# Kernel tuning notes

Measured on AMD Instinct MI355X. Metric: run time of the kernel, lower is better.

The kernel has to match this reference:

```python
import jax, jax.numpy as jnp
import numpy as np

N_NODES = 100000
N_EDGES = 640000
EMB = 128
BATCH = 16384
N_REL = 2
HIDDEN = [128, 64, 32]
LN_EPS = 1e-5
NORM_EPS = 1e-12


def setup_inputs() -> dict:
    key = jax.random.key(0)
    ks = jax.random.split(key, 24)
    inp = {}
    inp["user_indices"] = jax.random.randint(ks[0], (BATCH,), 0, N_NODES)
    inp["item_indices"] = jax.random.randint(ks[1], (BATCH,), 0, N_NODES)
    inp["edge_index"] = jax.random.randint(ks[2], (2, N_EDGES), 0, N_NODES)
    inp["edge_type"] = jax.random.randint(ks[3], (N_EDGES,), 0, N_REL)
    inp["edge_weight"] = jax.random.uniform(ks[4], (N_EDGES,), dtype=jnp.float32)
    # parameters
    s = 1.0 / np.sqrt(EMB)
    inp["embedding"] = jax.random.normal(ks[5], (N_NODES, EMB), jnp.float32) * 0.02
    inp["w1_rel"] = jax.random.normal(ks[6], (N_REL, EMB, EMB), jnp.float32) * s
    inp["w1_root"] = jax.random.normal(ks[7], (EMB, EMB), jnp.float32) * s
    inp["b1"] = jnp.zeros((EMB,), jnp.float32)
    inp["ln_g"] = jnp.ones((EMB,), jnp.float32)
    inp["ln_b"] = jnp.zeros((EMB,), jnp.float32)
    inp["w2_rel"] = jax.random.normal(ks[8], (N_REL, EMB, EMB), jnp.float32) * s
    inp["w2_root"] = jax.random.normal(ks[9], (EMB, EMB), jnp.float32) * s
    inp["b2"] = jnp.zeros((EMB,), jnp.float32)
    dims = [2 * EMB] + HIDDEN
    for i in range(len(HIDDEN)):
        inp[f"mlp_w{i}"] = jax.random.normal(ks[10 + i], (dims[i], dims[i + 1]), jnp.float32) / np.sqrt(dims[i])
        inp[f"mlp_b{i}"] = jnp.zeros((dims[i + 1],), jnp.float32)
    d_out = HIDDEN[-1] + EMB
    inp["out_w"] = jax.random.normal(ks[20], (d_out, 1), jnp.float32) / np.sqrt(d_out)
    inp["out_b"] = jnp.zeros((1,), jnp.float32)
    return inp


def rgcn_layer(x, edge_index, edge_type, edge_weight, w_rel, w_root, bias):
    # x: [N, D]; edge_index: [2, E]; per-relation linear on gathered source feats,
    # weighted scatter-add into destination nodes, plus root transform + bias.
    src, dst = edge_index[0], edge_index[1]
    x_j = x[src]  # [E, D] gather
    msg = jnp.zeros((x_j.shape[0], w_rel.shape[2]), x.dtype)
    for r in range(w_rel.shape[0]):  # small fixed relation count
        msg = msg + jnp.where((edge_type == r)[:, None], x_j @ w_rel[r], 0.0)
    msg = msg * edge_weight[:, None]
    agg = jax.ops.segment_sum(msg, dst, num_segments=x.shape[0])
    return agg + x @ w_root + bias


def layer_norm(x, g, b):
    mu = jnp.mean(x, axis=-1, keepdims=True)
    var = jnp.mean(jnp.square(x - mu), axis=-1, keepdims=True)
    return (x - mu) * jax.lax.rsqrt(var + LN_EPS) * g + b


def l2_normalize(x):
    n = jnp.sqrt(jnp.sum(jnp.square(x), axis=-1, keepdims=True))
    return x / jnp.maximum(n, NORM_EPS)


def reference(user_indices, item_indices, edge_index, edge_type, edge_weight,
              embedding, w1_rel, w1_root, b1, ln_g, ln_b, w2_rel, w2_root, b2,
              mlp_w0, mlp_b0, mlp_w1, mlp_b1, mlp_w2, mlp_b2, out_w, out_b):
    x = embedding  # embedding(arange(N)) == full table
    x = rgcn_layer(x, edge_index, edge_type, edge_weight, w1_rel, w1_root, b1)
    x = jax.nn.relu(x)
    # dropout is identity in eval mode
    x = layer_norm(x, ln_g, ln_b)
    x = rgcn_layer(x, edge_index, edge_type, edge_weight, w2_rel, w2_root, b2)

    u = x[user_indices]  # [B, D]
    v = x[item_indices]
    gmf = l2_normalize(u) * l2_normalize(v)  # [B, D]
    h = jnp.concatenate([u, v], axis=-1)  # [B, 2D]
    for w, b in ((mlp_w0, mlp_b0), (mlp_w1, mlp_b1), (mlp_w2, mlp_b2)):
        h = jax.nn.relu(h @ w + b)
    final = jnp.concatenate([gmf, h], axis=-1)  # [B, D + 32]
    score = jax.nn.sigmoid(final @ out_w + out_b)
    return jnp.squeeze(score, axis=-1)
```

## Files before the change

kernel.cpp:

```cpp
#include <hip/hip_runtime.h>
#include <cstddef>
#include <cstdint>

#define N_NODES 100000
#define N_EDGES 640000
#define EMBD    128
#define NBATCH  16384
#define CHUNK   1024
#define NCHUNK  ((N_NODES + CHUNK - 1) / CHUNK)

typedef short bf16x8 __attribute__((ext_vector_type(8)));
typedef float f32x4  __attribute__((ext_vector_type(4)));

__device__ __forceinline__ unsigned pack_split(float x) {
    unsigned u  = __float_as_uint(x);
    unsigned hi = (u + 0x7fffu + ((u >> 16) & 1u)) & 0xffff0000u;
    float    lo = x - __uint_as_float(hi);
    unsigned ul = __float_as_uint(lo);
    unsigned lw = ((ul + 0x7fffu + ((ul >> 16) & 1u)) >> 16) & 0xffffu;
    return hi | lw;
}
__device__ __forceinline__ float unpack_split(unsigned u) {
    return __uint_as_float(u & 0xffff0000u) + __uint_as_float(u << 16);
}
__device__ __forceinline__ float bf2f(unsigned short h) {
    return __uint_as_float((unsigned)h << 16);
}

__global__ __launch_bounds__(256) void pack_hist(
    const float* __restrict__ emb, unsigned* __restrict__ xp,
    unsigned short* __restrict__ xh,
    const int* __restrict__ ei, int* __restrict__ cursor, int n2, int E)
{
    const int j = blockIdx.x * 256 + threadIdx.x;
    if (j < n2) {
        const float2 v = ((const float2*)emb)[j];
        const unsigned p0 = pack_split(v.x);
        const unsigned p1 = pack_split(v.y);
        ((uint2*)xp)[j] = make_uint2(p0, p1);
        if (xh) ((unsigned*)xh)[j] = (p0 >> 16) | (p1 & 0xffff0000u);
    }
    if (j < E) atomicAdd(&cursor[ei[E + j]], 1);
}

__global__ __launch_bounds__(256) void scan_local(
    int* __restrict__ cursor, int* __restrict__ bsum, int n)
{
    __shared__ int part[256];
    const int t    = threadIdx.x;
    const int base = blockIdx.x * CHUNK + t * 4;
    int v[4];
    int s = 0;
#pragma unroll
    for (int i = 0; i < 4; ++i) {
        const int idx = base + i;
        v[i] = (idx < n) ? cursor[idx] : 0;
        s += v[i];
    }
    part[t] = s;
    __syncthreads();
    for (int off = 1; off < 256; off <<= 1) {
        const int add = (t >= off) ? part[t - off] : 0;
        __syncthreads();
        part[t] += add;
        __syncthreads();
    }
    if (t == 255) bsum[blockIdx.x] = part[255];
    int run = (t == 0) ? 0 : part[t - 1];
#pragma unroll
    for (int i = 0; i < 4; ++i) {
        const int idx = base + i;
        if (idx < n) { cursor[idx] = run; run += v[i]; }
    }
}

__global__ __launch_bounds__(256) void scan_add(
    int* __restrict__ cursor, const int* __restrict__ bsum, int n)
{
    __shared__ int red[256];
    const int t = threadIdx.x;
    const int b = blockIdx.x;
    red[t] = (t < b && t < NCHUNK) ? bsum[t] : 0;
    __syncthreads();
    for (int off = 128; off > 0; off >>= 1) {
        if (t < off) red[t] += red[t + off];
        __syncthreads();
    }
    const int off_ = red[0];
    const int base = b * CHUNK + t * 4;
#pragma unroll
    for (int i = 0; i < 4; ++i) {
        const int idx = base + i;
        if (idx < n) cursor[idx] += off_;
    }
}

__global__ __launch_bounds__(256) void bucket_kernel(
    const int* __restrict__ ei, const int* __restrict__ et,
    const float* __restrict__ ew, int* __restrict__ cursor,
    int2* __restrict__ srec, int E)
{
    const int e = blockIdx.x * 256 + threadIdx.x;
    if (e >= E) return;
    const int src = ei[e];
    const int dst = ei[E + e];
    const int r   = et[e];
    const int pos = atomicAdd(&cursor[dst], 1);
    srec[pos] = make_int2(src | (r << 17), __float_as_int(ew[e]));
}

template <bool HI>
__global__ __launch_bounds__(256) void accum_csr(
    const unsigned* __restrict__ xp, const unsigned short* __restrict__ xh,
    const int2* __restrict__ srec, const int* __restrict__ cursor,
    unsigned* __restrict__ Ap, int N)
{
    const int wid  = blockIdx.x * 4 + (threadIdx.x >> 6);
    const int lane = threadIdx.x & 63;
    const int s = (wid == 0) ? 0 : cursor[wid - 1];
    const int e = cursor[wid];

    float ax = 0.f, ay = 0.f, bx = 0.f, by = 0.f;

    auto fetch = [&](int src, float& vx, float& vy) {
        if (HI) {
            const unsigned g = ((const unsigned*)(xh + (size_t)src * EMBD))[lane];
            vx = bf2f((unsigned short)(g & 0xffffu));
            vy = bf2f((unsigned short)(g >> 16));
        } else {
            const uint2 g = ((const uint2*)(xp + (size_t)src * EMBD))[lane];
            vx = unpack_split(g.x);
            vy = unpack_split(g.y);
        }
    };

    int i = s;
    for (; i + 3 < e; i += 4) {
        const int2 r0 = srec[i];
        const int2 r1 = srec[i + 1];
        const int2 r2 = srec[i + 2];
        const int2 r3 = srec[i + 3];
        float x0, y0, x1, y1, x2v, y2v, x3, y3;
        fetch(r0.x & 0x1FFFF, x0, y0);
        fetch(r1.x & 0x1FFFF, x1, y1);
        fetch(r2.x & 0x1FFFF, x2v, y2v);
        fetch(r3.x & 0x1FFFF, x3, y3);
        const float w0 = __int_as_float(r0.y);
        const float w1 = __int_as_float(r1.y);
        const float w2 = __int_as_float(r2.y);
        const float w3 = __int_as_float(r3.y);
        if (r0.x & (1 << 17)) { bx += x0 * w0;  by += y0 * w0; }
        else                  { ax += x0 * w0;  ay += y0 * w0; }
        if (r1.x & (1 << 17)) { bx += x1 * w1;  by += y1 * w1; }
        else                  { ax += x1 * w1;  ay += y1 * w1; }
        if (r2.x & (1 << 17)) { bx += x2v * w2; by += y2v * w2; }
        else                  { ax += x2v * w2; ay += y2v * w2; }
        if (r3.x & (1 << 17)) { bx += x3 * w3;  by += y3 * w3; }
        else                  { ax += x3 * w3;  ay += y3 * w3; }
    }
    for (; i < e; ++i) {
        const int2 r0 = srec[i];
        float x0, y0;
        fetch(r0.x & 0x1FFFF, x0, y0);
        const float w0 = __int_as_float(r0.y);
        if (r0.x & (1 << 17)) { bx += x0 * w0; by += y0 * w0; }
        else                  { ax += x0 * w0; ay += y0 * w0; }
    }
    ((uint2*)(Ap + (size_t)wid * EMBD))[lane]       = make_uint2(pack_split(ax), pack_split(ay));
    ((uint2*)(Ap + ((size_t)N + wid) * EMBD))[lane] = make_uint2(pack_split(bx), pack_split(by));
}

__global__ __launch_bounds__(256) void gemm_mfma(
    const unsigned* __restrict__ S0, const unsigned* __restrict__ S1,
    const unsigned* __restrict__ S2,
    const float* __restrict__ wrel, const float* __restrict__ wroot,
    const float* __restrict__ bias, const float* __restrict__ lng,
    const float* __restrict__ lnb, void* __restrict__ outv,
    unsigned short* __restrict__ ohi,
    int M, int do_ln)
{
    __shared__ unsigned short AsH[128 * 40], AsL[128 * 40];
    __shared__ unsigned short BsH[128 * 40], BsL[128 * 40];
    __shared__ float lnbuf[2][128][2];

    const int t    = threadIdx.x;
    const int wave = t >> 6;
    const int lane = t & 63;
    const int q    = lane >> 4;
    const int n    = lane & 15;
    const int wrow = wave & 1;
    const int wcol = wave >> 1;
    const int m0   = blockIdx.x * 128;

    const int arow  = t >> 1;
    const int ahalf = t & 1;
    const int bcol  = t & 127;
    const int bkh   = t >> 7;

    f32x4 acc[4][4];
#pragma unroll
    for (int rt = 0; rt < 4; ++rt)
#pragma unroll
        for (int ct = 0; ct < 4; ++ct)
            acc[rt][ct] = (f32x4){0.f, 0.f, 0.f, 0.f};

    uint4 au0, au1, au2, au3;
    auto loadA = [&](int kc) {
        const unsigned* Sp = (kc < 4) ? S0 : (kc < 8) ? S1 : S2;
        const int rg = m0 + arow;
        if (rg < M) {
            const unsigned* p = Sp + (size_t)rg * EMBD + (kc & 3) * 32 + ahalf * 16;
            au0 = *(const uint4*)(p);
            au1 = *(const uint4*)(p + 4);
            au2 = *(const uint4*)(p + 8);
            au3 = *(const uint4*)(p + 12);
        } else {
            au0 = au1 = au2 = au3 = make_uint4(0u, 0u, 0u, 0u);
        }
    };

    loadA(0);

    for (int kc = 0; kc < 12; ++kc) {
        __syncthreads();

        {
            const unsigned uu[16] = {au0.x, au0.y, au0.z, au0.w,
                                     au1.x, au1.y, au1.z, au1.w,
                                     au2.x, au2.y, au2.z, au2.w,
                                     au3.x, au3.y, au3.z, au3.w};
            unsigned dh[8], dl[8];
#pragma unroll
            for (int i = 0; i < 8; ++i) {
                const unsigned e0 = uu[2 * i], e1 = uu[2 * i + 1];
                dh[i] = (e1 & 0xffff0000u) | (e0 >> 16);
                dl[i] = (e1 << 16) | (e0 & 0xffffu);
            }
            uint4* pH = (uint4*)(AsH + arow * 40 + ahalf * 16);
            uint4* pL = (uint4*)(AsL + arow * 40 + ahalf * 16);
            pH[0] = make_uint4(dh[0], dh[1], dh[2], dh[3]);
            pH[1] = make_uint4(dh[4], dh[5], dh[6], dh[7]);
            pL[0] = make_uint4(dl[0], dl[1], dl[2], dl[3]);
            pL[1] = make_uint4(dl[4], dl[5], dl[6], dl[7]);
        }

        if (kc < 11) loadA(kc + 1);

        {
            const float* Wsrc = (kc < 8) ? (wrel + (size_t)kc * 32 * EMBD)
                                         : (wroot + (size_t)(kc - 8) * 32 * EMBD);
            unsigned pk[16];
#pragma unroll
            for (int j = 0; j < 16; ++j)
                pk[j] = pack_split(Wsrc[(size_t)(bkh * 16 + j) * EMBD + bcol]);
            unsigned dh[8], dl[8];
#pragma unroll
            for (int i = 0; i < 8; ++i) {
                const unsigned e0 = pk[2 * i], e1 = pk[2 * i + 1];
                dh[i] = (e1 & 0xffff0000u) | (e0 >> 16);
                dl[i] = (e1 << 16) | (e0 & 0xffffu);
            }
            uint4* pH = (uint4*)(BsH + bcol * 40 + bkh * 16);
            uint4* pL = (uint4*)(BsL + bcol * 40 + bkh * 16);
            pH[0] = make_uint4(dh[0], dh[1], dh[2], dh[3]);
            pH[1] = make_uint4(dh[4], dh[5], dh[6], dh[7]);
            pL[0] = make_uint4(dl[0], dl[1], dl[2], dl[3]);
            pL[1] = make_uint4(dl[4], dl[5], dl[6], dl[7]);
        }
        __syncthreads();

        bf16x8 ah[4], al[4];
#pragma unroll
        for (int rt = 0; rt < 4; ++rt) {
            const int r = wrow * 64 + rt * 16 + n;
            ah[rt] = *(const bf16x8*)&AsH[r * 40 + q * 8];
            al[rt] = *(const bf16x8*)&AsL[r * 40 + q * 8];
        }
#pragma unroll
        for (int ct = 0; ct < 4; ++ct) {
            const int c = wcol * 64 + ct * 16 + n;
            const bf16x8 bh = *(const bf16x8*)&BsH[c * 40 + q * 8];
            const bf16x8 bl = *(const bf16x8*)&BsL[c * 40 + q * 8];
#pragma unroll
            for (int rt = 0; rt < 4; ++rt) {
                acc[rt][ct] = __builtin_amdgcn_mfma_f32_16x16x32_bf16(ah[rt], bh, acc[rt][ct], 0, 0, 0);
                acc[rt][ct] = __builtin_amdgcn_mfma_f32_16x16x32_bf16(ah[rt], bl, acc[rt][ct], 0, 0, 0);
                acc[rt][ct] = __builtin_amdgcn_mfma_f32_16x16x32_bf16(al[rt], bh, acc[rt][ct], 0, 0, 0);
            }
        }
    }

    float bb[4], gg[4], tb[4];
#pragma unroll
    for (int ct = 0; ct < 4; ++ct) {
        const int c = wcol * 64 + ct * 16 + n;
        bb[ct] = bias[c];
        gg[ct] = do_ln ? lng[c] : 0.f;
        tb[ct] = do_ln ? lnb[c] : 0.f;
    }

    if (do_ln) {
#pragma unroll
        for (int rt = 0; rt < 4; ++rt)
#pragma unroll
            for (int r = 0; r < 4; ++r) {
                float s = 0.f, sq = 0.f;
#pragma unroll
                for (int ct = 0; ct < 4; ++ct) {
                    float v = acc[rt][ct][r] + bb[ct];
                    v = fmaxf(v, 0.f);
                    acc[rt][ct][r] = v;
                    s += v; sq += v * v;
                }
#pragma unroll
                for (int off = 1; off < 16; off <<= 1) {
                    s  += __shfl_xor(s,  off, 64);
                    sq += __shfl_xor(sq, off, 64);
                }
                if (n == 0) {
                    const int row = wrow * 64 + rt * 16 + q * 4 + r;
                    lnbuf[wcol][row][0] = s;
                    lnbuf[wcol][row][1] = sq;
                }
            }
        __syncthreads();
        unsigned* outp = (unsigned*)outv;
#pragma unroll
        for (int rt = 0; rt < 4; ++rt)
#pragma unroll
            for (int r = 0; r < 4; ++r) {
                const int row = wrow * 64 + rt * 16 + q * 4 + r;
                const int rg  = m0 + row;
                const float s    = lnbuf[0][row][0] + lnbuf[1][row][0];
                const float sq   = lnbuf[0][row][1] + lnbuf[1][row][1];
                const float mu   = s * (1.0f / 128.0f);
                const float var  = sq * (1.0f / 128.0f) - mu * mu;
                const float rstd = rsqrtf(var + 1e-5f);
                if (rg < M) {
#pragma unroll
                    for (int ct = 0; ct < 4; ++ct) {
                        const int c = wcol * 64 + ct * 16 + n;
                        const float v = (acc[rt][ct][r] - mu) * rstd * gg[ct] + tb[ct];
                        const unsigned p = pack_split(v);
                        outp[(size_t)rg * EMBD + c] = p;
                        if (ohi) ohi[(size_t)rg * EMBD + c] = (unsigned short)(p >> 16);
                    }
                }
            }
    } else {
        float* outp = (float*)outv;
#pragma unroll
        for (int rt = 0; rt < 4; ++rt)
#pragma unroll
            for (int r = 0; r < 4; ++r) {
                const int rg = m0 + wrow * 64 + rt * 16 + q * 4 + r;
                if (rg < M) {
#pragma unroll
                    for (int ct = 0; ct < 4; ++ct) {
                        const int c = wcol * 64 + ct * 16 + n;
                        outp[(size_t)rg * EMBD + c] = acc[rt][ct][r] + bb[ct];
                    }
                }
            }
    }
}

__global__ __launch_bounds__(256) void head_kernel(
    const float* __restrict__ x2, const int* __restrict__ ui, const int* __restrict__ vi,
    const float* __restrict__ mw0, const float* __restrict__ mb0,
    const float* __restrict__ mw1, const float* __restrict__ mb1,
    const float* __restrict__ mw2, const float* __restrict__ mb2,
    const float* __restrict__ ow, const float* __restrict__ ob,
    float* __restrict__ out, int B)
{
    __shared__ float h0[16][256];
    __shared__ float h1[16][128];
    __shared__ float h2[16][64];
    __shared__ float h3[16][32];
    __shared__ float ps_u[16][16], ps_v[16][16];
    __shared__ float inv_nunv[16];
    __shared__ float pg[16][16], ph[16][16];

    const int t   = threadIdx.x;
    const int bb0 = blockIdx.x * 16;

    for (int r = 0; r < 16; ++r) {
        const int b   = bb0 + r;
        const int idx = (t < 128) ? ui[b] : vi[b];
        const int c   = t & 127;
        h0[r][t] = x2[(size_t)idx * EMBD + c];
    }
    __syncthreads();

    {
        const int row = t >> 4, sub = t & 15;
        float su = 0.f, sv = 0.f;
#pragma unroll
        for (int k = 0; k < 8; ++k) {
            const float a = h0[row][sub + 16 * k];       su += a * a;
            const float b = h0[row][128 + sub + 16 * k]; sv += b * b;
        }
        ps_u[row][sub] = su; ps_v[row][sub] = sv;
    }
    __syncthreads();
    if (t < 16) {
        float su = 0.f, sv = 0.f;
#pragma unroll
        for (int k = 0; k < 16; ++k) { su += ps_u[t][k]; sv += ps_v[t][k]; }
        const float nu = fmaxf(sqrtf(su), 1e-12f);
        const float nv = fmaxf(sqrtf(sv), 1e-12f);
        inv_nunv[t] = 1.0f / (nu * nv);
    }
    __syncthreads();

    {
        const int c = t & 127, rr = t >> 7;
        float acc[8];
#pragma unroll
        for (int j = 0; j < 8; ++j) acc[j] = 0.f;
        for (int i = 0; i < 256; i += 4) {
            const float w0 = mw0[(i + 0) * 128 + c];
            const float w1 = mw0[(i + 1) * 128 + c];
            const float w2 = mw0[(i + 2) * 128 + c];
            const float w3 = mw0[(i + 3) * 128 + c];
#pragma unroll
            for (int j = 0; j < 8; ++j) {
                const float4 a = *(const float4*)&h0[rr * 8 + j][i];
                acc[j] += a.x * w0 + a.y * w1 + a.z * w2 + a.w * w3;
            }
        }
        const float bv = mb0[c];
#pragma unroll
        for (int j = 0; j < 8; ++j) h1[rr * 8 + j][c] = fmaxf(acc[j] + bv, 0.f);
    }
    __syncthreads();

    {
        const int c = t & 63, g = t >> 6;
        float acc[4] = {0.f, 0.f, 0.f, 0.f};
        for (int i = 0; i < 128; i += 4) {
            const float w0 = mw1[(i + 0) * 64 + c];
            const float w1 = mw1[(i + 1) * 64 + c];
            const float w2 = mw1[(i + 2) * 64 + c];
            const float w3 = mw1[(i + 3) * 64 + c];
#pragma unroll
            for (int j = 0; j < 4; ++j) {
                const float4 a = *(const float4*)&h1[g * 4 + j][i];
                acc[j] += a.x * w0 + a.y * w1 + a.z * w2 + a.w * w3;
            }
        }
        const float bv = mb1[c];
#pragma unroll
        for (int j = 0; j < 4; ++j) h2[g * 4 + j][c] = fmaxf(acc[j] + bv, 0.f);
    }
    __syncthreads();

    {
        const int c = t & 31, g = t >> 5;
        float acc[2] = {0.f, 0.f};
        for (int i = 0; i < 64; i += 4) {
            const float w0 = mw2[(i + 0) * 32 + c];
            const float w1 = mw2[(i + 1) * 32 + c];
            const float w2 = mw2[(i + 2) * 32 + c];
            const float w3 = mw2[(i + 3) * 32 + c];
#pragma unroll
            for (int j = 0; j < 2; ++j) {
                const float4 a = *(const float4*)&h2[g * 2 + j][i];
                acc[j] += a.x * w0 + a.y * w1 + a.z * w2 + a.w * w3;
            }
        }
        const float bv = mb2[c];
#pragma unroll
        for (int j = 0; j < 2; ++j) h3[g * 2 + j][c] = fmaxf(acc[j] + bv, 0.f);
    }
    __syncthreads();

    {
        const int row = t >> 4, sub = t & 15;
        float pgv = 0.f;
#pragma unroll
        for (int k = 0; k < 8; ++k) {
            const int c = sub + 16 * k;
            pgv += h0[row][c] * h0[row][128 + c] * ow[c];
        }
        const float phv = h3[row][sub]      * ow[128 + sub]
                        + h3[row][sub + 16] * ow[144 + sub];
        pg[row][sub] = pgv; ph[row][sub] = phv;
    }
    __syncthreads();
    if (t < 16) {
        float sg = 0.f, sh = 0.f;
#pragma unroll
        for (int k = 0; k < 16; ++k) { sg += pg[t][k]; sh += ph[t][k]; }
        const float z = sg * inv_nunv[t] + sh + ob[0];
        out[bb0 + t] = 1.0f / (1.0f + expf(-z));
    }
}

extern "C" void kernel_launch(void* const* d_in, const int* in_sizes, int n_in,
                              void* d_out, int out_size, void* d_ws, size_t ws_size,
                              hipStream_t stream)
{
    const int*   ui      = (const int*)d_in[0];
    const int*   vi      = (const int*)d_in[1];
    const int*   ei      = (const int*)d_in[2];
    const int*   et      = (const int*)d_in[3];
    const float* ew      = (const float*)d_in[4];
    const float* emb     = (const float*)d_in[5];
    const float* w1_rel  = (const float*)d_in[6];
    const float* w1_root = (const float*)d_in[7];
    const float* b1      = (const float*)d_in[8];
    const float* ln_g    = (const float*)d_in[9];
    const float* ln_b    = (const float*)d_in[10];
    const float* w2_rel  = (const float*)d_in[11];
    const float* w2_root = (const float*)d_in[12];
    const float* b2      = (const float*)d_in[13];
    const float* mw0     = (const float*)d_in[14];
    const float* mb0     = (const float*)d_in[15];
    const float* mw1     = (const float*)d_in[16];
    const float* mb1     = (const float*)d_in[17];
    const float* mw2     = (const float*)d_in[18];
    const float* mb2     = (const float*)d_in[19];
    const float* ow      = (const float*)d_in[20];
    const float* ob      = (const float*)d_in[21];
    float* out = (float*)d_out;

    const int N = N_NODES, E = N_EDGES, B = NBATCH;

    unsigned* Ap = (unsigned*)d_ws;
    unsigned* xp = Ap + (size_t)2 * N * EMBD;
    int2*   srec   = (int2*)(xp + (size_t)N * EMBD);
    int*    cursor = (int*)(srec + E);
    int*    bsum   = cursor + N;
    unsigned short* xhi = (unsigned short*)(bsum + NCHUNK);

    const size_t need_hi = (size_t)((char*)(xhi + (size_t)N * EMBD) - (char*)d_ws);
    const bool have_hi = (ws_size >= need_hi);
    unsigned short* xh = have_hi ? xhi : nullptr;

    float* x2 = (float*)Ap;

    hipMemsetAsync(cursor, 0, N * sizeof(int), stream);
    pack_hist<<<(N * EMBD / 2 + 255) / 256, 256, 0, stream>>>(
        emb, xp, xh, ei, cursor, N * EMBD / 2, E);

    scan_local<<<NCHUNK, 256, 0, stream>>>(cursor, bsum, N);
    scan_add<<<NCHUNK, 256, 0, stream>>>(cursor, bsum, N);
    bucket_kernel<<<(E + 255) / 256, 256, 0, stream>>>(ei, et, ew, cursor, srec, E);

    const int ggrid = (N + 127) / 128;

    if (have_hi) accum_csr<true ><<<N / 4, 256, 0, stream>>>(xp, xh, srec, cursor, Ap, N);
    else         accum_csr<false><<<N / 4, 256, 0, stream>>>(xp, xh, srec, cursor, Ap, N);
    gemm_mfma<<<ggrid, 256, 0, stream>>>(
        Ap, Ap + (size_t)N * EMBD, xp,
        w1_rel, w1_root, b1, ln_g, ln_b, (void*)xp, xh, N, 1);

    if (have_hi) accum_csr<true ><<<N / 4, 256, 0, stream>>>(xp, xh, srec, cursor, Ap, N);
    else         accum_csr<false><<<N / 4, 256, 0, stream>>>(xp, xh, srec, cursor, Ap, N);
    gemm_mfma<<<ggrid, 256, 0, stream>>>(
        Ap, Ap + (size_t)N * EMBD, xp,
        w2_rel, w2_root, b2, nullptr, nullptr, (void*)x2, nullptr, N, 0);

    head_kernel<<<B / 16, 256, 0, stream>>>(
        x2, ui, vi, mw0, mb0, mw1, mb1, mw2, mb2, ow, ob, out, B);
}
```

Baseline: 482.6 us.

## Compute second RGCN layer only for nodes referenced by the batch

Builds a deduplicated list of the user and item node indices during the pack/histogram pass. The second layer's aggregation and GEMM then run only over those nodes rather than all nodes, using a row-indirection table inside the GEMM. The head only reads those rows, so the output is unchanged, but the list order comes from atomics and the extra flag and list buffers need more workspace.

```diff
diff --git a/kernel.cpp b/kernel.cpp
--- a/kernel.cpp
+++ b/kernel.cpp
@@ -30,7 +30,10 @@
 __global__ __launch_bounds__(256) void pack_hist(
     const float* __restrict__ emb, unsigned* __restrict__ xp,
     unsigned short* __restrict__ xh,
-    const int* __restrict__ ei, int* __restrict__ cursor, int n2, int E)
+    const int* __restrict__ ei, int* __restrict__ cursor,
+    const int* __restrict__ ui, const int* __restrict__ vi,
+    int* __restrict__ flag, int* __restrict__ nlist, int* __restrict__ count,
+    int n2, int E)
 {
     const int j = blockIdx.x * 256 + threadIdx.x;
     if (j < n2) {
@@ -41,6 +44,11 @@
         if (xh) ((unsigned*)xh)[j] = (p0 >> 16) | (p1 & 0xffff0000u);
     }
     if (j < E) atomicAdd(&cursor[ei[E + j]], 1);
+    if (flag && j < 2 * NBATCH) {
+        const int idx = (j < NBATCH) ? ui[j] : vi[j - NBATCH];
+        if (atomicExch(&flag[idx], 1) == 0)
+            nlist[atomicAdd(count, 1)] = idx;
+    }
 }
 
 __global__ __launch_bounds__(256) void scan_local(
@@ -109,62 +117,101 @@
     srec[pos] = make_int2(src | (r << 17), __float_as_int(ew[e]));
 }
 
-template <bool HI>
-__global__ __launch_bounds__(256) void accum_csr(
-    const unsigned* __restrict__ xp, const unsigned short* __restrict__ xh,
-    const int2* __restrict__ srec, const int* __restrict__ cursor,
-    unsigned* __restrict__ Ap, int N)
-{
-    const int wid  = blockIdx.x * 4 + (threadIdx.x >> 6);
-    const int lane = threadIdx.x & 63;
+__device__ __forceinline__ void accum_node(
+    const unsigned short* __restrict__ xh, const int2* __restrict__ srec,
+    const int* __restrict__ cursor, unsigned* __restrict__ Ap,
+    int wid, int lane, int N)
+{
     const int s = (wid == 0) ? 0 : cursor[wid - 1];
     const int e = cursor[wid];
 
     float ax = 0.f, ay = 0.f, bx = 0.f, by = 0.f;
-
-    auto fetch = [&](int src, float& vx, float& vy) {
-        if (HI) {
-            const unsigned g = ((const unsigned*)(xh + (size_t)src * EMBD))[lane];
-            vx = bf2f((unsigned short)(g & 0xffffu));
-            vy = bf2f((unsigned short)(g >> 16));
-        } else {
-            const uint2 g = ((const uint2*)(xp + (size_t)src * EMBD))[lane];
-            vx = unpack_split(g.x);
-            vy = unpack_split(g.y);
-        }
-    };
-
     int i = s;
     for (; i + 3 < e; i += 4) {
         const int2 r0 = srec[i];
         const int2 r1 = srec[i + 1];
         const int2 r2 = srec[i + 2];
         const int2 r3 = srec[i + 3];
-        float x0, y0, x1, y1, x2v, y2v, x3, y3;
-        fetch(r0.x & 0x1FFFF, x0, y0);
-        fetch(r1.x & 0x1FFFF, x1, y1);
-        fetch(r2.x & 0x1FFFF, x2v, y2v);
-        fetch(r3.x & 0x1FFFF, x3, y3);
+        const unsigned g0 = ((const unsigned*)(xh + (size_t)(r0.x & 0x1FFFF) * EMBD))[lane];
+        const unsigned g1 = ((const unsigned*)(xh + (size_t)(r1.x & 0x1FFFF) * EMBD))[lane];
+        const unsigned g2 = ((const unsigned*)(xh + (size_t)(r2.x & 0x1FFFF) * EMBD))[lane];
+        const unsigned g3 = ((const unsigned*)(xh + (size_t)(r3.x & 0x1FFFF) * EMBD))[lane];
         const float w0 = __int_as_float(r0.y);
         const float w1 = __int_as_float(r1.y);
         const float w2 = __int_as_float(r2.y);
         const float w3 = __int_as_float(r3.y);
-        if (r0.x & (1 << 17)) { bx += x0 * w0;  by += y0 * w0; }
-        else                  { ax += x0 * w0;  ay += y0 * w0; }
-        if (r1.x & (1 << 17)) { bx += x1 * w1;  by += y1 * w1; }
-        else                  { ax += x1 * w1;  ay += y1 * w1; }
-        if (r2.x & (1 << 17)) { bx += x2v * w2; by += y2v * w2; }
-        else                  { ax += x2v * w2; ay += y2v * w2; }
-        if (r3.x & (1 << 17)) { bx += x3 * w3;  by += y3 * w3; }
-        else                  { ax += x3 * w3;  ay += y3 * w3; }
+        {
+            const float vx = bf2f((unsigned short)(g0 & 0xffffu));
+            const float vy = bf2f((unsigned short)(g0 >> 16));
+            if (r0.x & (1 << 17)) { bx += vx * w0; by += vy * w0; }
+            else                  { ax += vx * w0; ay += vy * w0; }
+        }
+        {
+            const float vx = bf2f((unsigned short)(g1 & 0xffffu));
+            const float vy = bf2f((unsigned short)(g1 >> 16));
+            if (r1.x & (1 << 17)) { bx += vx * w1; by += vy * w1; }
+            else                  { ax += vx * w1; ay += vy * w1; }
+        }
+        {
+            const float vx = bf2f((unsigned short)(g2 & 0xffffu));
+            const float vy = bf2f((unsigned short)(g2 >> 16));
+            if (r2.x & (1 << 17)) { bx += vx * w2; by += vy * w2; }
+            else                  { ax += vx * w2; ay += vy * w2; }
+        }
+        {
+            const float vx = bf2f((unsigned short)(g3 & 0xffffu));
+            const float vy = bf2f((unsigned short)(g3 >> 16));
+            if (r3.x & (1 << 17)) { bx += vx * w3; by += vy * w3; }
+            else                  { ax += vx * w3; ay += vy * w3; }
+        }
     }
     for (; i < e; ++i) {
         const int2 r0 = srec[i];
-        float x0, y0;
-        fetch(r0.x & 0x1FFFF, x0, y0);
+        const unsigned g0 = ((const unsigned*)(xh + (size_t)(r0.x & 0x1FFFF) * EMBD))[lane];
         const float w0 = __int_as_float(r0.y);
-        if (r0.x & (1 << 17)) { bx += x0 * w0; by += y0 * w0; }
-        else                  { ax += x0 * w0; ay += y0 * w0; }
+        const float vx = bf2f((unsigned short)(g0 & 0xffffu));
+        const float vy = bf2f((unsigned short)(g0 >> 16));
+        if (r0.x & (1 << 17)) { bx += vx * w0; by += vy * w0; }
+        else                  { ax += vx * w0; ay += vy * w0; }
+    }
+    ((uint2*)(Ap + (size_t)wid * EMBD))[lane]       = make_uint2(pack_split(ax), pack_split(ay));
+    ((uint2*)(Ap + ((size_t)N + wid) * EMBD))[lane] = make_uint2(pack_split(bx), pack_split(by));
+}
+
+__global__ __launch_bounds__(256) void accum_csr(
+    const unsigned short* __restrict__ xh, const int2* __restrict__ srec,
+    const int* __restrict__ cursor, unsigned* __restrict__ Ap, int N)
+{
+    const int wid = blockIdx.x * 4 + (threadIdx.x >> 6);
+    accum_node(xh, srec, cursor, Ap, wid, threadIdx.x & 63, N);
+}
+
+__global__ __launch_bounds__(256) void accum_csr_list(
+    const unsigned short* __restrict__ xh, const int2* __restrict__ srec,
+    const int* __restrict__ cursor, const int* __restrict__ nlist,
+    const int* __restrict__ count, unsigned* __restrict__ Ap, int N)
+{
+    const int wi = blockIdx.x * 4 + (threadIdx.x >> 6);
+    if (wi >= *count) return;
+    accum_node(xh, srec, cursor, Ap, nlist[wi], threadIdx.x & 63, N);
+}
+
+__global__ __launch_bounds__(256) void accum_csr_full(
+    const unsigned* __restrict__ xp, const int2* __restrict__ srec,
+    const int* __restrict__ cursor, unsigned* __restrict__ Ap, int N)
+{
+    const int wid  = blockIdx.x * 4 + (threadIdx.x >> 6);
+    const int lane = threadIdx.x & 63;
+    const int s = (wid == 0) ? 0 : cursor[wid - 1];
+    const int e = cursor[wid];
+    float ax = 0.f, ay = 0.f, bx = 0.f, by = 0.f;
+    for (int i = s; i < e; ++i) {
+        const int2 r0 = srec[i];
+        const uint2 g = ((const uint2*)(xp + (size_t)(r0.x & 0x1FFFF) * EMBD))[lane];
+        const float w0 = __int_as_float(r0.y);
+        const float vx = unpack_split(g.x), vy = unpack_split(g.y);
+        if (r0.x & (1 << 17)) { bx += vx * w0; by += vy * w0; }
+        else                  { ax += vx * w0; ay += vy * w0; }
     }
     ((uint2*)(Ap + (size_t)wid * EMBD))[lane]       = make_uint2(pack_split(ax), pack_split(ay));
     ((uint2*)(Ap + ((size_t)N + wid) * EMBD))[lane] = make_uint2(pack_split(bx), pack_split(by));
@@ -177,11 +224,13 @@
     const float* __restrict__ bias, const float* __restrict__ lng,
     const float* __restrict__ lnb, void* __restrict__ outv,
     unsigned short* __restrict__ ohi,
+    const int* __restrict__ rowlist, const int* __restrict__ rowcnt,
     int M, int do_ln)
 {
     __shared__ unsigned short AsH[128 * 40], AsL[128 * 40];
     __shared__ unsigned short BsH[128 * 40], BsL[128 * 40];
     __shared__ float lnbuf[2][128][2];
+    __shared__ int rows[128];
 
     const int t    = threadIdx.x;
     const int wave = t >> 6;
@@ -192,6 +241,14 @@
     const int wcol = wave >> 1;
     const int m0   = blockIdx.x * 128;
 
+    const int cnt = rowcnt ? *rowcnt : M;
+    if (m0 >= cnt) return;
+    if (t < 128) {
+        const int rr = m0 + t;
+        rows[t] = (rr < cnt) ? (rowlist ? rowlist[rr] : rr) : -1;
+    }
+    __syncthreads();
+
     const int arow  = t >> 1;
     const int ahalf = t & 1;
     const int bcol  = t & 127;
@@ -207,9 +264,9 @@
     uint4 au0, au1, au2, au3;
     auto loadA = [&](int kc) {
         const unsigned* Sp = (kc < 4) ? S0 : (kc < 8) ? S1 : S2;
-        const int rg = m0 + arow;
-        if (rg < M) {
-            const unsigned* p = Sp + (size_t)rg * EMBD + (kc & 3) * 32 + ahalf * 16;
+        const int node = rows[arow];
+        if (node >= 0) {
+            const unsigned* p = Sp + (size_t)node * EMBD + (kc & 3) * 32 + ahalf * 16;
             au0 = *(const uint4*)(p);
             au1 = *(const uint4*)(p + 4);
             au2 = *(const uint4*)(p + 8);
@@ -329,21 +386,21 @@
         for (int rt = 0; rt < 4; ++rt)
 #pragma unroll
             for (int r = 0; r < 4; ++r) {
-                const int row = wrow * 64 + rt * 16 + q * 4 + r;
-                const int rg  = m0 + row;
+                const int row  = wrow * 64 + rt * 16 + q * 4 + r;
+                const int node = rows[row];
                 const float s    = lnbuf[0][row][0] + lnbuf[1][row][0];
                 const float sq   = lnbuf[0][row][1] + lnbuf[1][row][1];
                 const float mu   = s * (1.0f / 128.0f);
                 const float var  = sq * (1.0f / 128.0f) - mu * mu;
                 const float rstd = rsqrtf(var + 1e-5f);
-                if (rg < M) {
+                if (node >= 0) {
 #pragma unroll
                     for (int ct = 0; ct < 4; ++ct) {
                         const int c = wcol * 64 + ct * 16 + n;
                         const float v = (acc[rt][ct][r] - mu) * rstd * gg[ct] + tb[ct];
                         const unsigned p = pack_split(v);
-                        outp[(size_t)rg * EMBD + c] = p;
-                        if (ohi) ohi[(size_t)rg * EMBD + c] = (unsigned short)(p >> 16);
+                        outp[(size_t)node * EMBD + c] = p;
+                        if (ohi) ohi[(size_t)node * EMBD + c] = (unsigned short)(p >> 16);
                     }
                 }
             }
@@ -353,12 +410,12 @@
         for (int rt = 0; rt < 4; ++rt)
 #pragma unroll
             for (int r = 0; r < 4; ++r) {
-                const int rg = m0 + wrow * 64 + rt * 16 + q * 4 + r;
-                if (rg < M) {
+                const int node = rows[wrow * 64 + rt * 16 + q * 4 + r];
+                if (node >= 0) {
 #pragma unroll
                     for (int ct = 0; ct < 4; ++ct) {
                         const int c = wcol * 64 + ct * 16 + n;
-                        outp[(size_t)rg * EMBD + c] = acc[rt][ct][r] + bb[ct];
+                        outp[(size_t)node * EMBD + c] = acc[rt][ct][r] + bb[ct];
                     }
                 }
             }
@@ -531,18 +588,24 @@
     unsigned* xp = Ap + (size_t)2 * N * EMBD;
     int2*   srec   = (int2*)(xp + (size_t)N * EMBD);
     int*    cursor = (int*)(srec + E);
-    int*    bsum   = cursor + N;
+    int*    flag   = cursor + N;
+    int*    count  = flag + N;
+    int*    bsum   = count + 1;
     unsigned short* xhi = (unsigned short*)(bsum + NCHUNK);
-
-    const size_t need_hi = (size_t)((char*)(xhi + (size_t)N * EMBD) - (char*)d_ws);
-    const bool have_hi = (ws_size >= need_hi);
-    unsigned short* xh = have_hi ? xhi : nullptr;
+    int*    nlist  = (int*)(xhi + (size_t)N * EMBD);
+
+    const size_t need_ext = (size_t)((char*)(nlist + 2 * NBATCH) - (char*)d_ws);
+    const bool have_ext = (ws_size >= need_ext);
+    unsigned short* xh = have_ext ? xhi : nullptr;
 
     float* x2 = (float*)Ap;
 
-    hipMemsetAsync(cursor, 0, N * sizeof(int), stream);
+    if (have_ext) hipMemsetAsync(cursor, 0, (size_t)(2 * N + 1) * sizeof(int), stream);
+    else          hipMemsetAsync(cursor, 0, (size_t)N * sizeof(int), stream);
     pack_hist<<<(N * EMBD / 2 + 255) / 256, 256, 0, stream>>>(
-        emb, xp, xh, ei, cursor, N * EMBD / 2, E);
+        emb, xp, xh, ei, cursor,
+        ui, vi, have_ext ? flag : nullptr, nlist, count,
+        N * EMBD / 2, E);
 
     scan_local<<<NCHUNK, 256, 0, stream>>>(cursor, bsum, N);
     scan_add<<<NCHUNK, 256, 0, stream>>>(cursor, bsum, N);
@@ -550,17 +613,31 @@
 
     const int ggrid = (N + 127) / 128;
 
-    if (have_hi) accum_csr<true ><<<N / 4, 256, 0, stream>>>(xp, xh, srec, cursor, Ap, N);
-    else         accum_csr<false><<<N / 4, 256, 0, stream>>>(xp, xh, srec, cursor, Ap, N);
-    gemm_mfma<<<ggrid, 256, 0, stream>>>(
-        Ap, Ap + (size_t)N * EMBD, xp,
-        w1_rel, w1_root, b1, ln_g, ln_b, (void*)xp, xh, N, 1);
-
-    if (have_hi) accum_csr<true ><<<N / 4, 256, 0, stream>>>(xp, xh, srec, cursor, Ap, N);
-    else         accum_csr<false><<<N / 4, 256, 0, stream>>>(xp, xh, srec, cursor, Ap, N);
-    gemm_mfma<<<ggrid, 256, 0, stream>>>(
-        Ap, Ap + (size_t)N * EMBD, xp,
-        w2_rel, w2_root, b2, nullptr, nullptr, (void*)x2, nullptr, N, 0);
+    if (have_ext) {
+        accum_csr<<<N / 4, 256, 0, stream>>>(xh, srec, cursor, Ap, N);
+        gemm_mfma<<<ggrid, 256, 0, stream>>>(
+            Ap, Ap + (size_t)N * EMBD, xp,
+            w1_rel, w1_root, b1, ln_g, ln_b, (void*)xp, xh,
+            nullptr, nullptr, N, 1);
+
+        accum_csr_list<<<(2 * NBATCH) / 4, 256, 0, stream>>>(
+            xh, srec, cursor, nlist, count, Ap, N);
+        gemm_mfma<<<(2 * NBATCH + 127) / 128, 256, 0, stream>>>(
+            Ap, Ap + (size_t)N * EMBD, xp,
+            w2_rel, w2_root, b2, nullptr, nullptr, (void*)x2, nullptr,
+            nlist, count, N, 0);
+    } else {
+        accum_csr_full<<<N / 4, 256, 0, stream>>>(xp, srec, cursor, Ap, N);
+        gemm_mfma<<<ggrid, 256, 0, stream>>>(
+            Ap, Ap + (size_t)N * EMBD, xp,
+            w1_rel, w1_root, b1, ln_g, ln_b, (void*)xp, nullptr,
+            nullptr, nullptr, N, 1);
+        accum_csr_full<<<N / 4, 256, 0, stream>>>(xp, srec, cursor, Ap, N);
+        gemm_mfma<<<ggrid, 256, 0, stream>>>(
+            Ap, Ap + (size_t)N * EMBD, xp,
+            w2_rel, w2_root, b2, nullptr, nullptr, (void*)x2, nullptr,
+            nullptr, nullptr, N, 0);
+    }
 
     head_kernel<<<B / 16, 256, 0, stream>>>(
         x2, ui, vi, mw0, mb0, mw1, mb1, mw2, mb2, ow, ob, out, B);
```

Result: faster. 429.0 us (-11.1%).
